# Optimization experiments

Measured on AMD Instinct MI355X. Metric: run time of the kernel, lower is better.

The kernel has to match this reference:

```python
import jax, jax.numpy as jnp
import numpy as np

N_FEATURES = 128
POISSON_LAMBDA = 2.0
B = 500000


def setup_inputs() -> dict:
    key = jax.random.key(0)
    kx, km = jax.random.split(key)
    x = jax.random.normal(kx, (B, N_FEATURES), dtype=jnp.float32)
    mask = (jax.random.uniform(km, (B, N_FEATURES)) > 0.1).astype(jnp.float32)
    return {"x": x, "mask": mask}


def reference(x, mask):
    """Vectorized equivalent of the per-row Python loop:
    per row, draw n ~ Poisson(lambda) clipped to [0, F-1]; if the row has
    >1 valid features, mask n = min(n, n_valid-1) uniformly-random valid
    features (set to 0 in both x and the validity mask).
    Uniform random subset selection is done by ranking random scores:
    valid positions get U(0,1) scores, invalid get -1; the n highest-scoring
    valid positions form a uniform random n-subset of the valid indices.
    """
    Bn, F = x.shape
    kp, ku = jax.random.split(jax.random.key(42))
    valid = mask > 0.5
    n_valid = valid.sum(axis=1)  # (B,) int
    n = jnp.clip(jax.random.poisson(kp, POISSON_LAMBDA, (Bn,)), 0, F - 1)
    n = jnp.where(n_valid > 1, jnp.minimum(n, n_valid - 1), 0)  # (B,)
    scores = jnp.where(valid, jax.random.uniform(ku, (Bn, F)), -1.0)
    order = jnp.argsort(-scores, axis=1)          # columns sorted by descending score
    ranks = jnp.argsort(order, axis=1)            # rank of each column (0 = highest score)
    drop = (ranks < n[:, None]) & valid           # n random valid positions per row
    random_mask = jnp.where(drop, 0.0, 1.0).astype(x.dtype)
    return x * random_mask, mask * random_mask
```

## Files before the change

kernel.cpp:

```cpp
#include <hip/hip_runtime.h>
#include <cstdint>
#include <math.h>


#define DH __host__ __device__ __forceinline__

DH uint32_t rotl32(uint32_t v, uint32_t r) { return (v << r) | (v >> (32u - r)); }

DH void tf2x32(uint32_t k0, uint32_t k1, uint32_t x0, uint32_t x1,
               uint32_t& o0, uint32_t& o1) {
  const uint32_t k2 = k0 ^ k1 ^ 0x1BD11BDAu;
  x0 += k0; x1 += k1;
  x0 += x1; x1 = rotl32(x1, 13); x1 ^= x0;
  x0 += x1; x1 = rotl32(x1, 15); x1 ^= x0;
  x0 += x1; x1 = rotl32(x1, 26); x1 ^= x0;
  x0 += x1; x1 = rotl32(x1,  6); x1 ^= x0;
  x0 += k1; x1 += k2 + 1u;
  x0 += x1; x1 = rotl32(x1, 17); x1 ^= x0;
  x0 += x1; x1 = rotl32(x1, 29); x1 ^= x0;
  x0 += x1; x1 = rotl32(x1, 16); x1 ^= x0;
  x0 += x1; x1 = rotl32(x1, 24); x1 ^= x0;
  x0 += k2; x1 += k0 + 2u;
  x0 += x1; x1 = rotl32(x1, 13); x1 ^= x0;
  x0 += x1; x1 = rotl32(x1, 15); x1 ^= x0;
  x0 += x1; x1 = rotl32(x1, 26); x1 ^= x0;
  x0 += x1; x1 = rotl32(x1,  6); x1 ^= x0;
  x0 += k0; x1 += k1 + 3u;
  x0 += x1; x1 = rotl32(x1, 17); x1 ^= x0;
  x0 += x1; x1 = rotl32(x1, 29); x1 ^= x0;
  x0 += x1; x1 = rotl32(x1, 16); x1 ^= x0;
  x0 += x1; x1 = rotl32(x1, 24); x1 ^= x0;
  x0 += k1; x1 += k2 + 4u;
  x0 += x1; x1 = rotl32(x1, 13); x1 ^= x0;
  x0 += x1; x1 = rotl32(x1, 15); x1 ^= x0;
  x0 += x1; x1 = rotl32(x1, 26); x1 ^= x0;
  x0 += x1; x1 = rotl32(x1,  6); x1 ^= x0;
  x0 += k2; x1 += k0 + 5u;
  o0 = x0; o1 = x1;
}

__device__ __forceinline__ float u01(uint32_t bits) {
  return __uint_as_float((bits >> 9) | 0x3f800000u) - 1.0f;
}

struct PoisKeys { uint32_t s0[32]; uint32_t s1[32]; };

__global__ __launch_bounds__(256) void pois_n_kernel(
    uint8_t* __restrict__ nout, int B, PoisKeys pk) {
  const int row = (int)(blockIdx.x * 256u + threadIdx.x);
  if (row >= B) return;
  float lp = 0.0f;
  int k = 0;
  for (int it = 0; it < 32; ++it) {
    if (lp <= -2.0f) break;
    uint32_t b0, b1;
    tf2x32(pk.s0[it], pk.s1[it], 0u, (uint32_t)row, b0, b1);
    ++k;
    lp += (float)log((double)u01(b0 ^ b1));
  }
  nout[row] = (uint8_t)(k - 1);
}

__global__ __launch_bounds__(256) void rfm_main(
    const float* __restrict__ x, const float* __restrict__ mask,
    const uint8_t* __restrict__ nraw, float* __restrict__ out,
    int B, int G, uint32_t ku0, uint32_t ku1) {
  const int tid = (int)threadIdx.x;
  const int li  = tid & 15;
  const int g0  = (int)(blockIdx.x * 16u) + (tid >> 4);
  if (g0 >= B) return;
  const size_t NF = (size_t)B * 128u;
  const size_t lo = (size_t)(li * 8);

  {
  }
  size_t pbase = (size_t)g0 * 128u + lo;
  float4 cma = *(const float4*)(mask + pbase);
  float4 cmb = *(const float4*)(mask + pbase + 4);
  int cn = (int)nraw[g0];

  for (int r = g0; r < B; ) {
    const size_t base = (size_t)r * 128u + lo;
    const float4 xa = *(const float4*)(x + base);
    const float4 xb = *(const float4*)(x + base + 4);
    const int rn = r + G;
    float4 nma, nmb;
    int nn = 0;
    if (rn < B) {
      const size_t nb = (size_t)rn * 128u + lo;
      nma = *(const float4*)(mask + nb);
      nmb = *(const float4*)(mask + nb + 4);
      nn = (int)nraw[rn];
    } else {
      nma = cma; nmb = cmb;
    }

    float mv[8] = {cma.x, cma.y, cma.z, cma.w, cmb.x, cmb.y, cmb.z, cmb.w};
    uint32_t dropbits = 0u;

    if (__any(cn > 0)) {
      float s[8];
      int nv = 0;
      const uint32_t idx0 = (uint32_t)r * 128u + (uint32_t)(li * 8);
#pragma unroll
      for (int j = 0; j < 8; ++j) {
        uint32_t b0, b1;
        tf2x32(ku0, ku1, 0u, idx0 + (uint32_t)j, b0, b1);
        const bool valid = mv[j] > 0.5f;
        s[j] = valid ? u01(b0 ^ b1) : -1.0f;
        nv += valid ? 1 : 0;
      }
#pragma unroll
      for (int off = 8; off; off >>= 1) nv += __shfl_xor(nv, off);

      const int nd = (nv > 1) ? min(cn, nv - 1) : 0;

      for (int t = 0; t < nd; ++t) {
        float bs = s[0];
        int bj = 0;
#pragma unroll
        for (int j = 1; j < 8; ++j) {
          if (s[j] > bs) { bs = s[j]; bj = j; }
        }
        int bc = (li << 3) + bj;
#pragma unroll
        for (int off = 8; off; off >>= 1) {
          const float os = __shfl_xor(bs, off);
          const int   oc = __shfl_xor(bc, off);
          if (os > bs || (os == bs && oc < bc)) { bs = os; bc = oc; }
        }
        const bool own = (bc >> 3) == li;
        const int  lj  = bc & 7;
#pragma unroll
        for (int j = 0; j < 8; ++j) {
          if (own && lj == j) { s[j] = -2.0f; dropbits |= (1u << j); }
        }
      }
    }

    float xv[8] = {xa.x, xa.y, xa.z, xa.w, xb.x, xb.y, xb.z, xb.w};
#pragma unroll
    for (int j = 0; j < 8; ++j) {
      if ((dropbits >> j) & 1u) { xv[j] = 0.0f; mv[j] = 0.0f; }
    }
    float4 o;
    o.x = xv[0]; o.y = xv[1]; o.z = xv[2]; o.w = xv[3];
    *(float4*)(out + base) = o;
    o.x = xv[4]; o.y = xv[5]; o.z = xv[6]; o.w = xv[7];
    *(float4*)(out + base + 4) = o;
    o.x = mv[0]; o.y = mv[1]; o.z = mv[2]; o.w = mv[3];
    *(float4*)(out + NF + base) = o;
    o.x = mv[4]; o.y = mv[5]; o.z = mv[6]; o.w = mv[7];
    *(float4*)(out + NF + base + 4) = o;

    r = rn; cma = nma; cmb = nmb; cn = nn;
  }
}

__global__ __launch_bounds__(256) void rfm_fused(
    const float* __restrict__ x, const float* __restrict__ mask,
    float* __restrict__ out, int B,
    uint32_t ku0, uint32_t ku1, PoisKeys pk) {
  const int tid = (int)threadIdx.x;
  const int row = (int)blockIdx.x * 16 + (tid >> 4);
  if (row >= B) return;
  const int li = tid & 15;
  const int gb = (tid & 63) & 48;
  const size_t base = (size_t)row * 128u + (size_t)(li * 8);
  const size_t NF = (size_t)B * 128u;

  const float4 ma = *(const float4*)(mask + base);
  const float4 mb = *(const float4*)(mask + base + 4);
  const float4 xa = *(const float4*)(x + base);
  const float4 xb = *(const float4*)(x + base + 4);

  float lg;
  {
    uint32_t b0, b1;
    tf2x32(pk.s0[li], pk.s1[li], 0u, (uint32_t)row, b0, b1);
    lg = (float)log((double)u01(b0 ^ b1));
  }
  float lp = 0.0f;
  int k = 0;
#pragma unroll
  for (int j = 0; j < 8; ++j) {
    const float lj = __shfl(lg, gb + j);
    k += (lp > -2.0f) ? 1 : 0;
    lp += lj;
  }
  if (lp > -2.0f) {
#pragma unroll
    for (int j = 8; j < 16; ++j) {
      const float lj = __shfl(lg, gb + j);
      k += (lp > -2.0f) ? 1 : 0;
      lp += lj;
    }
    if (lp > -2.0f) {
      uint32_t c0, c1;
      const int i2 = 16 + (li & 7);
      tf2x32(pk.s0[i2], pk.s1[i2], 0u, (uint32_t)row, c0, c1);
      const float lg2 = (float)log((double)u01(c0 ^ c1));
#pragma unroll
      for (int j = 0; j < 8; ++j) {
        const float lj = __shfl(lg2, gb + j);
        k += (lp > -2.0f) ? 1 : 0;
        lp += lj;
      }
    }
  }
  int n = k - 1;

  float mv[8] = {ma.x, ma.y, ma.z, ma.w, mb.x, mb.y, mb.z, mb.w};
  float s[8];
  int nv = 0;
  const uint32_t idx0 = (uint32_t)row * 128u + (uint32_t)(li * 8);
#pragma unroll
  for (int j = 0; j < 8; ++j) {
    uint32_t b0, b1;
    tf2x32(ku0, ku1, 0u, idx0 + (uint32_t)j, b0, b1);
    const bool valid = mv[j] > 0.5f;
    s[j] = valid ? u01(b0 ^ b1) : -1.0f;
    nv += valid ? 1 : 0;
  }
#pragma unroll
  for (int off = 8; off; off >>= 1) nv += __shfl_xor(nv, off);
  n = (nv > 1) ? min(n, nv - 1) : 0;

  uint32_t dropbits = 0u;
  for (int t = 0; t < n; ++t) {
    float bs = s[0];
    int bj = 0;
#pragma unroll
    for (int j = 1; j < 8; ++j) {
      if (s[j] > bs) { bs = s[j]; bj = j; }
    }
    int bc = (li << 3) + bj;
#pragma unroll
    for (int off = 8; off; off >>= 1) {
      const float os = __shfl_xor(bs, off);
      const int   oc = __shfl_xor(bc, off);
      if (os > bs || (os == bs && oc < bc)) { bs = os; bc = oc; }
    }
    const bool own = (bc >> 3) == li;
    const int  lj  = bc & 7;
#pragma unroll
    for (int j = 0; j < 8; ++j) {
      if (own && lj == j) { s[j] = -2.0f; dropbits |= (1u << j); }
    }
  }

  float xv[8] = {xa.x, xa.y, xa.z, xa.w, xb.x, xb.y, xb.z, xb.w};
#pragma unroll
  for (int j = 0; j < 8; ++j) {
    if ((dropbits >> j) & 1u) { xv[j] = 0.0f; mv[j] = 0.0f; }
  }
  float4 o;
  o.x = xv[0]; o.y = xv[1]; o.z = xv[2]; o.w = xv[3];
  *(float4*)(out + base) = o;
  o.x = xv[4]; o.y = xv[5]; o.z = xv[6]; o.w = xv[7];
  *(float4*)(out + base + 4) = o;
  o.x = mv[0]; o.y = mv[1]; o.z = mv[2]; o.w = mv[3];
  *(float4*)(out + NF + base) = o;
  o.x = mv[4]; o.y = mv[5]; o.z = mv[6]; o.w = mv[7];
  *(float4*)(out + NF + base + 4) = o;
}

extern "C" void kernel_launch(void* const* d_in, const int* in_sizes, int n_in,
                              void* d_out, int out_size, void* d_ws, size_t ws_size,
                              hipStream_t stream) {
  const float* x    = (const float*)d_in[0];
  const float* mask = (const float*)d_in[1];
  float* out = (float*)d_out;

  const int B = in_sizes[0] / 128;

  uint32_t kp0, kp1, ku0, ku1;
  tf2x32(0u, 42u, 0u, 0u, kp0, kp1);
  tf2x32(0u, 42u, 0u, 1u, ku0, ku1);

  PoisKeys pk;
  {
    uint32_t r0 = kp0, r1 = kp1;
    for (int it = 0; it < 32; ++it) {
      uint32_t s0, s1, t0, t1;
      tf2x32(r0, r1, 0u, 1u, s0, s1);
      tf2x32(r0, r1, 0u, 0u, t0, t1);
      pk.s0[it] = s0; pk.s1[it] = s1;
      r0 = t0; r1 = t1;
    }
  }

  if (ws_size < (size_t)B) {
    rfm_fused<<<(B + 15) / 16, 256, 0, stream>>>(x, mask, out, B, ku0, ku1, pk);
    return;
  }

  uint8_t* nraw = (uint8_t*)d_ws;
  pois_n_kernel<<<(B + 255) / 256, 256, 0, stream>>>(nraw, B, pk);

  int blocks = (B + 15) / 16;
  if (blocks > 2048) blocks = 2048;
  const int G = blocks * 16;
  rfm_main<<<blocks, 256, 0, stream>>>(x, mask, nraw, out, B, G, ku0, ku1);
}
```

Measured before the change: 249.3 us.

## Sort rows by drop need within blocks, one row per group, integer scores

Replaces the grid-stride persistent loop with one-shot blocks of 1024 threads covering 64 rows. Within each block, rows are permuted so that rows with n>0 come first. This clusters the expensive Threefry and selection work into the same wavefronts and lets rows with nothing to drop skip it entirely. Random scores are compared as 23-bit integers rather than floats, and the mask prefetch pipelining of the old loop is removed. The extra shared-memory ballot and permutation stage and the larger blocks add a sync and may lower latency hiding.

```diff
diff --git a/kernel.cpp b/kernel.cpp
--- a/kernel.cpp
+++ b/kernel.cpp
@@ -61,100 +61,104 @@
   nout[row] = (uint8_t)(k - 1);
 }
 
-__global__ __launch_bounds__(256) void rfm_main(
+__global__ __launch_bounds__(1024) void rfm_main(
     const float* __restrict__ x, const float* __restrict__ mask,
     const uint8_t* __restrict__ nraw, float* __restrict__ out,
-    int B, int G, uint32_t ku0, uint32_t ku1) {
+    int B, uint32_t ku0, uint32_t ku1) {
+  __shared__ uint8_t s_n[64];
+  __shared__ uint8_t s_perm[64];
   const int tid = (int)threadIdx.x;
-  const int li  = tid & 15;
-  const int g0  = (int)(blockIdx.x * 16u) + (tid >> 4);
-  if (g0 >= B) return;
+  const int rowBase = (int)(blockIdx.x * 64u);
+  const int nvalid = min(64, B - rowBase);
+
+  if (tid < 64) {
+    const bool vr = tid < nvalid;
+    const int n = vr ? (int)nraw[rowBase + tid] : 0;
+    s_n[tid] = (uint8_t)n;
+    const bool cls = vr && (n > 0);
+    const unsigned long long mh  = __ballot(cls);
+    const unsigned long long mvr = __ballot(vr);
+    const unsigned long long below = tid ? (~0ull >> (64 - tid)) : 0ull;
+    const int npos = __popcll(mh);
+    if (vr) {
+      const int slot = cls ? __popcll(mh & below)
+                           : npos + __popcll(mvr & (~mh) & below);
+      s_perm[slot] = (uint8_t)tid;
+    }
+  }
+  __syncthreads();
+
+  const int g = tid >> 4;
+  if (g >= nvalid) return;
+  const int li = tid & 15;
+  const int j = (int)s_perm[g];
+  const int row = rowBase + j;
+  int n = (int)s_n[j];
+
+  const size_t base = (size_t)row * 128u + (size_t)(li * 8);
   const size_t NF = (size_t)B * 128u;
-  const size_t lo = (size_t)(li * 8);
-
-  {
-  }
-  size_t pbase = (size_t)g0 * 128u + lo;
-  float4 cma = *(const float4*)(mask + pbase);
-  float4 cmb = *(const float4*)(mask + pbase + 4);
-  int cn = (int)nraw[g0];
-
-  for (int r = g0; r < B; ) {
-    const size_t base = (size_t)r * 128u + lo;
-    const float4 xa = *(const float4*)(x + base);
-    const float4 xb = *(const float4*)(x + base + 4);
-    const int rn = r + G;
-    float4 nma, nmb;
-    int nn = 0;
-    if (rn < B) {
-      const size_t nb = (size_t)rn * 128u + lo;
-      nma = *(const float4*)(mask + nb);
-      nmb = *(const float4*)(mask + nb + 4);
-      nn = (int)nraw[rn];
-    } else {
-      nma = cma; nmb = cmb;
-    }
-
-    float mv[8] = {cma.x, cma.y, cma.z, cma.w, cmb.x, cmb.y, cmb.z, cmb.w};
+
+  const float4 ma = *(const float4*)(mask + base);
+  const float4 mb = *(const float4*)(mask + base + 4);
+  const float4 xa = *(const float4*)(x + base);
+  const float4 xb = *(const float4*)(x + base + 4);
+  float mv[8] = {ma.x, ma.y, ma.z, ma.w, mb.x, mb.y, mb.z, mb.w};
+  float xv[8] = {xa.x, xa.y, xa.z, xa.w, xb.x, xb.y, xb.z, xb.w};
+
+  if (n > 0) {
+    uint32_t s[8];
+    int nv = 0;
+    const uint32_t idx0 = (uint32_t)row * 128u + (uint32_t)(li * 8);
+#pragma unroll
+    for (int jj = 0; jj < 8; ++jj) {
+      uint32_t b0, b1;
+      tf2x32(ku0, ku1, 0u, idx0 + (uint32_t)jj, b0, b1);
+      const bool valid = mv[jj] > 0.5f;
+      s[jj] = valid ? (((b0 ^ b1) >> 9) + 1u) : 0u;
+      nv += valid ? 1 : 0;
+    }
+#pragma unroll
+    for (int off = 8; off; off >>= 1) nv += __shfl_xor(nv, off);
+
+    n = (nv > 1) ? min(n, nv - 1) : 0;
+
     uint32_t dropbits = 0u;
-
-    if (__any(cn > 0)) {
-      float s[8];
-      int nv = 0;
-      const uint32_t idx0 = (uint32_t)r * 128u + (uint32_t)(li * 8);
-#pragma unroll
-      for (int j = 0; j < 8; ++j) {
-        uint32_t b0, b1;
-        tf2x32(ku0, ku1, 0u, idx0 + (uint32_t)j, b0, b1);
-        const bool valid = mv[j] > 0.5f;
-        s[j] = valid ? u01(b0 ^ b1) : -1.0f;
-        nv += valid ? 1 : 0;
+    for (int t = 0; t < n; ++t) {
+      uint32_t bs = s[0];
+      int bj = 0;
+#pragma unroll
+      for (int jj = 1; jj < 8; ++jj) {
+        if (s[jj] > bs) { bs = s[jj]; bj = jj; }
       }
-#pragma unroll
-      for (int off = 8; off; off >>= 1) nv += __shfl_xor(nv, off);
-
-      const int nd = (nv > 1) ? min(cn, nv - 1) : 0;
-
-      for (int t = 0; t < nd; ++t) {
-        float bs = s[0];
-        int bj = 0;
-#pragma unroll
-        for (int j = 1; j < 8; ++j) {
-          if (s[j] > bs) { bs = s[j]; bj = j; }
-        }
-        int bc = (li << 3) + bj;
-#pragma unroll
-        for (int off = 8; off; off >>= 1) {
-          const float os = __shfl_xor(bs, off);
-          const int   oc = __shfl_xor(bc, off);
-          if (os > bs || (os == bs && oc < bc)) { bs = os; bc = oc; }
-        }
-        const bool own = (bc >> 3) == li;
-        const int  lj  = bc & 7;
-#pragma unroll
-        for (int j = 0; j < 8; ++j) {
-          if (own && lj == j) { s[j] = -2.0f; dropbits |= (1u << j); }
-        }
+      int bc = (li << 3) + bj;
+#pragma unroll
+      for (int off = 8; off; off >>= 1) {
+        const uint32_t os = __shfl_xor(bs, off);
+        const int      oc = __shfl_xor(bc, off);
+        if (os > bs || (os == bs && oc < bc)) { bs = os; bc = oc; }
       }
-    }
-
-    float xv[8] = {xa.x, xa.y, xa.z, xa.w, xb.x, xb.y, xb.z, xb.w};
-#pragma unroll
-    for (int j = 0; j < 8; ++j) {
-      if ((dropbits >> j) & 1u) { xv[j] = 0.0f; mv[j] = 0.0f; }
-    }
-    float4 o;
-    o.x = xv[0]; o.y = xv[1]; o.z = xv[2]; o.w = xv[3];
-    *(float4*)(out + base) = o;
-    o.x = xv[4]; o.y = xv[5]; o.z = xv[6]; o.w = xv[7];
-    *(float4*)(out + base + 4) = o;
-    o.x = mv[0]; o.y = mv[1]; o.z = mv[2]; o.w = mv[3];
-    *(float4*)(out + NF + base) = o;
-    o.x = mv[4]; o.y = mv[5]; o.z = mv[6]; o.w = mv[7];
-    *(float4*)(out + NF + base + 4) = o;
-
-    r = rn; cma = nma; cmb = nmb; cn = nn;
-  }
+      const bool own = (bc >> 3) == li;
+      const int  lj  = bc & 7;
+#pragma unroll
+      for (int jj = 0; jj < 8; ++jj) {
+        if (own && lj == jj) { s[jj] = 0u; dropbits |= (1u << jj); }
+      }
+    }
+#pragma unroll
+    for (int jj = 0; jj < 8; ++jj) {
+      if ((dropbits >> jj) & 1u) { xv[jj] = 0.0f; mv[jj] = 0.0f; }
+    }
+  }
+
+  float4 o;
+  o.x = xv[0]; o.y = xv[1]; o.z = xv[2]; o.w = xv[3];
+  *(float4*)(out + base) = o;
+  o.x = xv[4]; o.y = xv[5]; o.z = xv[6]; o.w = xv[7];
+  *(float4*)(out + base + 4) = o;
+  o.x = mv[0]; o.y = mv[1]; o.z = mv[2]; o.w = mv[3];
+  *(float4*)(out + NF + base) = o;
+  o.x = mv[4]; o.y = mv[5]; o.z = mv[6]; o.w = mv[7];
+  *(float4*)(out + NF + base + 4) = o;
 }
 
 __global__ __launch_bounds__(256) void rfm_fused(
@@ -297,9 +301,5 @@
 
   uint8_t* nraw = (uint8_t*)d_ws;
   pois_n_kernel<<<(B + 255) / 256, 256, 0, stream>>>(nraw, B, pk);
-
-  int blocks = (B + 15) / 16;
-  if (blocks > 2048) blocks = 2048;
-  const int G = blocks * 16;
-  rfm_main<<<blocks, 256, 0, stream>>>(x, mask, nraw, out, B, G, ku0, ku1);
-}
+  rfm_main<<<(B + 63) / 64, 1024, 0, stream>>>(x, mask, nraw, out, B, ku0, ku1);
+}
```

Result: faster. 229.9 us (-7.8%).
